# Performance work log

Hardware: AMD Instinct MI355X
Metric: run time of the kernel (lower is better)

## Reference

```python
import jax, jax.numpy as jnp
import numpy as np

N, E, ND, ED, HID, H, L = 50000, 800000, 32, 16, 96, 4, 3
C = HID // H  # per-head channels = 24
NEG_SLOPE = 0.2
LN_EPS = 1e-5


def setup_inputs() -> dict:
    key = jax.random.key(0)
    ks = iter(jax.random.split(key, 40))
    def r(shape, s=0.05):
        return jax.random.normal(next(ks), shape, jnp.float32) * s
    return dict(
        x=r((N, ND), 1.0),
        edge_index=jax.random.randint(next(ks), (2, E), 0, N),
        edge_attr=r((E, ED), 1.0),
        proj_w=r((ND, HID)), proj_b=jnp.zeros((HID,), jnp.float32),
        lin_l_w=r((L, HID, HID)), lin_l_b=jnp.zeros((L, HID), jnp.float32),
        lin_r_w=r((L, HID, HID)), lin_r_b=jnp.zeros((L, HID), jnp.float32),
        lin_e_w=r((L, ED, HID)),
        att=r((L, H, C)),
        conv_b=jnp.zeros((L, HID), jnp.float32),
        ln_g=jnp.ones((L, HID), jnp.float32), ln_b=jnp.zeros((L, HID), jnp.float32),
        head_w1=r((HID, HID // 2)), head_b1=jnp.zeros((HID // 2,), jnp.float32),
        head_w2=r((HID // 2, 1)), head_b2=jnp.zeros((1,), jnp.float32),
    )


def _layernorm(h, g, b):
    mu = h.mean(-1, keepdims=True)
    var = ((h - mu) ** 2).mean(-1, keepdims=True)
    return (h - mu) / jnp.sqrt(var + LN_EPS) * g + b


def _gatv2(x, src, dst, edge_attr, Wl, bl, Wr, br, We, att, bias):
    # GATv2Conv (PyG semantics, eval mode): x_l = lin_l(x) for source, x_r = lin_r(x) for target
    xl = (x @ Wl + bl).reshape(N, H, C)
    xr = (x @ Wr + br).reshape(N, H, C)
    e = (edge_attr @ We).reshape(E, H, C)
    m = jax.nn.leaky_relu(xl[src] + xr[dst] + e, NEG_SLOPE)  # [E,H,C]
    alpha = (m * att).sum(-1)  # [E,H]
    # segment softmax over incoming edges of each target node
    amax = jax.ops.segment_max(alpha, dst, num_segments=N)  # [N,H]
    ea = jnp.exp(alpha - amax[dst])
    denom = jax.ops.segment_sum(ea, dst, num_segments=N)
    alpha = ea / (denom[dst] + 1e-16)
    out = jax.ops.segment_sum(xl[src] * alpha[..., None], dst, num_segments=N)
    return out.reshape(N, HID) + bias


def reference(x, edge_index, edge_attr, proj_w, proj_b, lin_l_w, lin_l_b, lin_r_w,
              lin_r_b, lin_e_w, att, conv_b, ln_g, ln_b, head_w1, head_b1, head_w2, head_b2):
    src, dst = edge_index[0], edge_index[1]
    h = x @ proj_w + proj_b
    for l in range(L):
        m = _gatv2(h, src, dst, edge_attr, lin_l_w[l], lin_l_b[l], lin_r_w[l],
                   lin_r_b[l], lin_e_w[l], att[l], conv_b[l])
        h = _layernorm(h + m, ln_g[l], ln_b[l])
    h = jax.nn.gelu(h @ head_w1 + head_b1, approximate=False)
    return (h @ head_w2 + head_b2).squeeze(-1)
```

## Files before the change

kernel.cpp:

```cpp
#include <hip/hip_runtime.h>

constexpr int N_NODES = 50000;
constexpr int N_EDGES = 800000;
constexpr int ND  = 32;
constexpr int ED  = 16;
constexpr int HID = 96;
constexpr int NLAYER = 3;

typedef unsigned short ushort_t;
typedef unsigned int uint_t;
typedef __attribute__((ext_vector_type(8))) short bf16x8;
typedef __attribute__((ext_vector_type(4))) float f32x4;

__device__ __forceinline__ float bf2f(ushort_t u) {
    union { float f; uint_t ui; } c; c.ui = ((uint_t)u) << 16; return c.f;
}
__device__ __forceinline__ ushort_t f2bf(float f) {
    uint_t u = __float_as_uint(f);
    return (ushort_t)((u + 0x7FFFu + ((u >> 16) & 1u)) >> 16);
}

__global__ void k_rank(const int* __restrict__ dst, int* __restrict__ cnt,
                       int* __restrict__ rank) {
    int e = blockIdx.x * 256 + threadIdx.x;
    if (e >= N_EDGES) return;
    rank[e] = atomicAdd(&cnt[dst[e]], 1);
}

__global__ void k_scan_block(const int* __restrict__ deg, int* __restrict__ rowptr,
                             int* __restrict__ bsum) {
    __shared__ int s[256];
    int i = blockIdx.x * 256 + threadIdx.x;
    int v = (i < N_NODES) ? deg[i] : 0;
    s[threadIdx.x] = v;
    __syncthreads();
    for (int off = 1; off < 256; off <<= 1) {
        int t = (threadIdx.x >= off) ? s[threadIdx.x - off] : 0;
        __syncthreads();
        s[threadIdx.x] += t;
        __syncthreads();
    }
    if (i < N_NODES) rowptr[i] = s[threadIdx.x] - v;
    if (threadIdx.x == 255) bsum[blockIdx.x] = s[255];
}

__global__ void k_scan_bsum(int* __restrict__ bsum, int nb) {
    __shared__ int s[256];
    int t = threadIdx.x;
    int v = (t < nb) ? bsum[t] : 0;
    s[t] = v;
    __syncthreads();
    for (int off = 1; off < 256; off <<= 1) {
        int tv = (t >= off) ? s[t - off] : 0;
        __syncthreads();
        s[t] += tv;
        __syncthreads();
    }
    if (t < nb) bsum[t] = s[t] - v;
}

__global__ void k_scan_add(int* __restrict__ rowptr, const int* __restrict__ bsum) {
    int i = blockIdx.x * 256 + threadIdx.x;
    if (i < N_NODES) rowptr[i] += bsum[blockIdx.x];
    if (i == 0) rowptr[N_NODES] = N_EDGES;
}

__global__ void k_place(const int* __restrict__ src, const int* __restrict__ dst,
                        const int* __restrict__ rank, const int* __restrict__ rowptr,
                        int2* __restrict__ csre) {
    int e = blockIdx.x * 256 + threadIdx.x;
    if (e >= N_EDGES) return;
    int p = rowptr[dst[e]] + rank[e];
    csre[p] = make_int2(src[e], e);
}

__global__ void k_gather(const int2* __restrict__ csre, const int* __restrict__ dstA,
                         const float* __restrict__ eattr, int* __restrict__ srcs,
                         int* __restrict__ pdst, ushort_t* __restrict__ ea) {
    int p = blockIdx.x * 256 + threadIdx.x;
    if (p >= N_EDGES) return;
    int2 se = csre[p];
    int e = se.y;
    srcs[p] = se.x;
    pdst[p] = dstA[e];
    const float4* er = (const float4*)(eattr + (size_t)e * ED);
    float4 v0 = er[0], v1 = er[1], v2 = er[2], v3 = er[3];
    uint4 w0, w1;
    w0.x = (uint_t)f2bf(v0.x) | ((uint_t)f2bf(v0.y) << 16);
    w0.y = (uint_t)f2bf(v0.z) | ((uint_t)f2bf(v0.w) << 16);
    w0.z = (uint_t)f2bf(v1.x) | ((uint_t)f2bf(v1.y) << 16);
    w0.w = (uint_t)f2bf(v1.z) | ((uint_t)f2bf(v1.w) << 16);
    w1.x = (uint_t)f2bf(v2.x) | ((uint_t)f2bf(v2.y) << 16);
    w1.y = (uint_t)f2bf(v2.z) | ((uint_t)f2bf(v2.w) << 16);
    w1.z = (uint_t)f2bf(v3.x) | ((uint_t)f2bf(v3.y) << 16);
    w1.w = (uint_t)f2bf(v3.z) | ((uint_t)f2bf(v3.w) << 16);
    uint4* ew = (uint4*)(ea + (size_t)p * ED);
    ew[0] = w0;
    ew[1] = w1;
}

__global__ __launch_bounds__(192) void k_proj(const float* __restrict__ x,
                                              const float* __restrict__ pw,
                                              const float* __restrict__ pb,
                                              float* __restrict__ h) {
    int t = threadIdx.x;
    int c = t % 96, half = t / 96;
    float wreg[ND];
#pragma unroll
    for (int k = 0; k < ND; k++) wreg[k] = pw[k * HID + c];
    float b = pb[c];
    int n0 = blockIdx.x * 16 + half * 8;
    for (int i = 0; i < 8; i += 2) {
        int na = n0 + i, nb = na + 1;
        const float4* xa = (const float4*)(x + (size_t)na * ND);
        const float4* xb = (const float4*)(x + (size_t)nb * ND);
        float accA = b, accB = b;
#pragma unroll
        for (int k4 = 0; k4 < ND / 4; k4++) {
            float4 va = xa[k4], vb = xb[k4];
            accA += va.x * wreg[4 * k4] + va.y * wreg[4 * k4 + 1] +
                    va.z * wreg[4 * k4 + 2] + va.w * wreg[4 * k4 + 3];
            accB += vb.x * wreg[4 * k4] + vb.y * wreg[4 * k4 + 1] +
                    vb.z * wreg[4 * k4 + 2] + vb.w * wreg[4 * k4 + 3];
        }
        h[(size_t)na * HID + c] = accA;
        h[(size_t)nb * HID + c] = accB;
    }
}

__global__ __launch_bounds__(256) void k_linlr_mfma(
    const float* __restrict__ h, const float* __restrict__ Wl,
    const float* __restrict__ bl, const float* __restrict__ Wr,
    const float* __restrict__ br, ushort_t* __restrict__ xl,
    ushort_t* __restrict__ xr) {
    __shared__ ushort_t sW[192 * 104];
    __shared__ float sB[192];
    int t = threadIdx.x;

    for (int idx = t; idx < 192 * 96; idx += 256) {
        int n = idx % 192, k = idx / 192;
        float v = (n < 96) ? Wl[k * 96 + n] : Wr[k * 96 + (n - 96)];
        sW[n * 104 + k] = f2bf(v);
    }
    if (t < 192) sB[t] = (t < 96) ? bl[t] : br[t - 96];
    __syncthreads();

    int wv = t >> 6, lane = t & 63;
    int m0 = blockIdx.x * 64 + wv * 16;
    if (m0 >= N_NODES) return;
    int m = lane & 15, quad = lane >> 4;

    bf16x8 afr[3];
    const float* hrow = h + (size_t)(m0 + m) * HID;
#pragma unroll
    for (int s = 0; s < 3; s++) {
        float4 v0 = *(const float4*)(hrow + s * 32 + quad * 8);
        float4 v1 = *(const float4*)(hrow + s * 32 + quad * 8 + 4);
        bf16x8 a;
        a[0] = (short)f2bf(v0.x); a[1] = (short)f2bf(v0.y);
        a[2] = (short)f2bf(v0.z); a[3] = (short)f2bf(v0.w);
        a[4] = (short)f2bf(v1.x); a[5] = (short)f2bf(v1.y);
        a[6] = (short)f2bf(v1.z); a[7] = (short)f2bf(v1.w);
        afr[s] = a;
    }

#pragma unroll
    for (int nt = 0; nt < 12; nt++) {
        int ch = nt * 16 + m;
        f32x4 acc = {0.f, 0.f, 0.f, 0.f};
#pragma unroll
        for (int s = 0; s < 3; s++) {
            bf16x8 bfr = *(const bf16x8*)(sW + (nt * 16 + m) * 104 + s * 32 + quad * 8);
            acc = __builtin_amdgcn_mfma_f32_16x16x32_bf16(afr[s], bfr, acc, 0, 0, 0);
        }
        float bias = sB[ch];
        ushort_t* dst = (ch < 96) ? (xl + (size_t)(m0 + quad * 4) * HID + ch)
                                  : (xr + (size_t)(m0 + quad * 4) * HID + (ch - 96));
#pragma unroll
        for (int r = 0; r < 4; r++)
            dst[(size_t)r * HID] = f2bf(acc[r] + bias);
    }
}

__global__ __launch_bounds__(256) void k_ev(
    const ushort_t* __restrict__ xlb, const ushort_t* __restrict__ xrb,
    const ushort_t* __restrict__ ea, const int* __restrict__ srcs,
    const int* __restrict__ pdst, const float* __restrict__ WeL,
    const float* __restrict__ attL, float* __restrict__ evf) {
    int wid = blockIdx.x * 4 + (threadIdx.x >> 6);
    int lane = threadIdx.x & 63;
    if (wid >= N_EDGES / 128) return;
    int col = lane & 15, quad = lane >> 4;
    int comp = col & 1, base = col >> 1;

    int2 sp = *(const int2*)(srcs + wid * 128 + 2 * lane);
    int2 dp = *(const int2*)(pdst + wid * 128 + 2 * lane);

    bf16x8 afr[6];
#pragma unroll
    for (int mc = 0; mc < 6; mc++) {
        bf16x8 a = {0, 0, 0, 0, 0, 0, 0, 0};
        if (quad < 2) {
            int ch = (col >> 2) * 24 + mc * 4 + (col & 3);
#pragma unroll
            for (int j = 0; j < 8; j++)
                a[j] = (short)f2bf(WeL[(quad * 8 + j) * HID + ch]);
        }
        afr[mc] = a;
    }
    float attr[6][4];
#pragma unroll
    for (int mc = 0; mc < 6; mc++)
#pragma unroll
        for (int r = 0; r < 4; r++)
            attr[mc][r] = attL[quad * 24 + mc * 4 + r];

    bf16x8 bfr[2];
    uint4 xq[2][3], rq[2][3];

    auto getsd = [&](int b, int& sv, int& dv) {
        int sl = b * 8 + base;
        int sx = __shfl(sp.x, sl), sy = __shfl(sp.y, sl);
        int dx = __shfl(dp.x, sl), dy = __shfl(dp.y, sl);
        sv = comp ? sy : sx;
        dv = comp ? dy : dx;
    };
    auto issue = [&](int b, int pp) {
        int sv, dv;
        getsd(b, sv, dv);
        int p = wid * 128 + b * 16 + col;
        bf16x8 z8 = {0, 0, 0, 0, 0, 0, 0, 0};
        bfr[pp] = (quad < 2) ? *(const bf16x8*)(ea + (size_t)p * ED + quad * 8) : z8;
        const uint4* xp = (const uint4*)(xlb + (size_t)sv * HID + quad * 24);
        const uint4* rp = (const uint4*)(xrb + (size_t)dv * HID + quad * 24);
#pragma unroll
        for (int i = 0; i < 3; i++) {
            xq[pp][i] = xp[i];
            rq[pp][i] = rp[i];
        }
    };

    issue(0, 0);
#pragma unroll
    for (int b = 0; b < 8; b++) {
        int pp = b & 1;
        if (b < 7) issue(b + 1, pp ^ 1);

        f32x4 zero4 = {0.f, 0.f, 0.f, 0.f};
        f32x4 d[6];
#pragma unroll
        for (int mc = 0; mc < 6; mc++)
            d[mc] = __builtin_amdgcn_mfma_f32_16x16x32_bf16(afr[mc], bfr[pp], zero4, 0, 0, 0);

        uint_t ux[12] = {xq[pp][0].x, xq[pp][0].y, xq[pp][0].z, xq[pp][0].w,
                         xq[pp][1].x, xq[pp][1].y, xq[pp][1].z, xq[pp][1].w,
                         xq[pp][2].x, xq[pp][2].y, xq[pp][2].z, xq[pp][2].w};
        uint_t ur[12] = {rq[pp][0].x, rq[pp][0].y, rq[pp][0].z, rq[pp][0].w,
                         rq[pp][1].x, rq[pp][1].y, rq[pp][1].z, rq[pp][1].w,
                         rq[pp][2].x, rq[pp][2].y, rq[pp][2].z, rq[pp][2].w};
        float logit = 0.f;
#pragma unroll
        for (int mc = 0; mc < 6; mc++) {
            uint_t aL = ux[2 * mc], aH = ux[2 * mc + 1];
            uint_t rL = ur[2 * mc], rH = ur[2 * mc + 1];
            float x0 = bf2f((ushort_t)(aL & 0xffff)), x1 = bf2f((ushort_t)(aL >> 16));
            float x2 = bf2f((ushort_t)(aH & 0xffff)), x3 = bf2f((ushort_t)(aH >> 16));
            float r0 = bf2f((ushort_t)(rL & 0xffff)), r1 = bf2f((ushort_t)(rL >> 16));
            float r2 = bf2f((ushort_t)(rH & 0xffff)), r3 = bf2f((ushort_t)(rH >> 16));
            float z0 = x0 + r0 + d[mc][0]; z0 = z0 > 0.f ? z0 : 0.2f * z0;
            float z1 = x1 + r1 + d[mc][1]; z1 = z1 > 0.f ? z1 : 0.2f * z1;
            float z2 = x2 + r2 + d[mc][2]; z2 = z2 > 0.f ? z2 : 0.2f * z2;
            float z3 = x3 + r3 + d[mc][3]; z3 = z3 > 0.f ? z3 : 0.2f * z3;
            logit += z0 * attr[mc][0] + z1 * attr[mc][1] +
                     z2 * attr[mc][2] + z3 * attr[mc][3];
        }
        int p = wid * 128 + b * 16 + col;
        evf[4 * p + quad] = __expf(logit);
    }
}

__global__ __launch_bounds__(256) void k_agg(
    const ushort_t* __restrict__ xlb, const float* __restrict__ evf,
    const int* __restrict__ srcs, const int* __restrict__ rowptr,
    const float* __restrict__ convb, const float* __restrict__ lng,
    const float* __restrict__ lnb, float* __restrict__ h) {
    int lane = threadIdx.x & 63;
    int node = blockIdx.x * 4 + (threadIdx.x >> 6);
    int slot = lane >> 3, q = lane & 7;
    int c0 = q * 12, head = q >> 1;
    int beg = rowptr[node], end = rowptr[node + 1];
    int cnt = (end - beg + 7) >> 3;

    float n[12];
#pragma unroll
    for (int j = 0; j < 12; j++) n[j] = 0.f;
    float den = 0.f;

    if (cnt > 0) {
        int p = beg + slot;
        bool v = p < end;
        int pc = v ? p : beg;
        int src = srcs[pc];
        float evv = evf[4 * pc + head];
        const ushort_t* xp = xlb + (size_t)src * HID + c0;
        uint2 A0 = *(const uint2*)(xp);
        uint2 A1 = *(const uint2*)(xp + 4);
        uint2 A2 = *(const uint2*)(xp + 8);
        for (int it = 0; it < cnt; ++it) {
            int pn = beg + (it + 1) * 8 + slot;
            bool vn = pn < end;
            int pcn = vn ? pn : beg;
            int srcn = srcs[pcn];
            float evn = evf[4 * pcn + head];
            const ushort_t* xpn = xlb + (size_t)srcn * HID + c0;
            uint2 B0 = *(const uint2*)(xpn);
            uint2 B1 = *(const uint2*)(xpn + 4);
            uint2 B2 = *(const uint2*)(xpn + 8);

            float e = v ? evv : 0.f;
            n[0]  += e * bf2f((ushort_t)(A0.x & 0xffff));
            n[1]  += e * bf2f((ushort_t)(A0.x >> 16));
            n[2]  += e * bf2f((ushort_t)(A0.y & 0xffff));
            n[3]  += e * bf2f((ushort_t)(A0.y >> 16));
            n[4]  += e * bf2f((ushort_t)(A1.x & 0xffff));
            n[5]  += e * bf2f((ushort_t)(A1.x >> 16));
            n[6]  += e * bf2f((ushort_t)(A1.y & 0xffff));
            n[7]  += e * bf2f((ushort_t)(A1.y >> 16));
            n[8]  += e * bf2f((ushort_t)(A2.x & 0xffff));
            n[9]  += e * bf2f((ushort_t)(A2.x >> 16));
            n[10] += e * bf2f((ushort_t)(A2.y & 0xffff));
            n[11] += e * bf2f((ushort_t)(A2.y >> 16));
            den += e;

            v = vn; evv = evn;
            A0 = B0; A1 = B1; A2 = B2;
        }
    }
#pragma unroll
    for (int j = 0; j < 12; j++) {
        n[j] += __shfl_xor(n[j], 8);
        n[j] += __shfl_xor(n[j], 16);
        n[j] += __shfl_xor(n[j], 32);
    }
    den += __shfl_xor(den, 8);
    den += __shfl_xor(den, 16);
    den += __shfl_xor(den, 32);

    size_t nb = (size_t)node * HID + c0;
    float inv = 1.f / (den + 1e-16f);
    float4 h0 = *(const float4*)(h + nb);
    float4 h1 = *(const float4*)(h + nb + 4);
    float4 h2 = *(const float4*)(h + nb + 8);
    float vv[12] = {h0.x, h0.y, h0.z, h0.w, h1.x, h1.y, h1.z, h1.w,
                    h2.x, h2.y, h2.z, h2.w};
    float sm = 0.f;
#pragma unroll
    for (int j = 0; j < 12; j++) {
        vv[j] += n[j] * inv + convb[c0 + j];
        sm += vv[j];
    }
    sm += __shfl_xor(sm, 1); sm += __shfl_xor(sm, 2); sm += __shfl_xor(sm, 4);
    float mu = sm * (1.f / 96.f);
    float sv = 0.f;
#pragma unroll
    for (int j = 0; j < 12; j++) {
        vv[j] -= mu;
        sv += vv[j] * vv[j];
    }
    sv += __shfl_xor(sv, 1); sv += __shfl_xor(sv, 2); sv += __shfl_xor(sv, 4);
    float rstd = rsqrtf(sv * (1.f / 96.f) + 1e-5f);
    if (slot == 0) {
        float o[12];
#pragma unroll
        for (int j = 0; j < 12; j++)
            o[j] = vv[j] * rstd * lng[c0 + j] + lnb[c0 + j];
        *(float4*)(h + nb)     = make_float4(o[0], o[1], o[2], o[3]);
        *(float4*)(h + nb + 4) = make_float4(o[4], o[5], o[6], o[7]);
        *(float4*)(h + nb + 8) = make_float4(o[8], o[9], o[10], o[11]);
    }
}

__global__ __launch_bounds__(256) void k_head_mfma(
    const float* __restrict__ h, const float* __restrict__ W1,
    const float* __restrict__ b1, const float* __restrict__ W2,
    const float* __restrict__ b2, float* __restrict__ out) {
    __shared__ ushort_t sW[48 * 104];
    __shared__ float sB1[48];
    __shared__ float sW2[48];
    int t = threadIdx.x;
    for (int idx = t; idx < 48 * 96; idx += 256) {
        int j = idx % 48, k = idx / 48;
        sW[j * 104 + k] = f2bf(W1[k * 48 + j]);
    }
    if (t < 48) { sB1[t] = b1[t]; sW2[t] = W2[t]; }
    __syncthreads();

    int wv = t >> 6, lane = t & 63;
    int m0 = blockIdx.x * 64 + wv * 16;
    if (m0 >= N_NODES) return;
    int col = lane & 15, quad = lane >> 4;

    bf16x8 afr[3];
    const float* hrow = h + (size_t)(m0 + col) * HID;
#pragma unroll
    for (int s = 0; s < 3; s++) {
        float4 v0 = *(const float4*)(hrow + s * 32 + quad * 8);
        float4 v1 = *(const float4*)(hrow + s * 32 + quad * 8 + 4);
        bf16x8 a;
        a[0] = (short)f2bf(v0.x); a[1] = (short)f2bf(v0.y);
        a[2] = (short)f2bf(v0.z); a[3] = (short)f2bf(v0.w);
        a[4] = (short)f2bf(v1.x); a[5] = (short)f2bf(v1.y);
        a[6] = (short)f2bf(v1.z); a[7] = (short)f2bf(v1.w);
        afr[s] = a;
    }

    const float inv_sqrt2 = 0.70710678118654752f;
    float y0 = 0.f, y1 = 0.f, y2 = 0.f, y3 = 0.f;
#pragma unroll
    for (int nt = 0; nt < 3; nt++) {
        f32x4 acc = {0.f, 0.f, 0.f, 0.f};
#pragma unroll
        for (int s = 0; s < 3; s++) {
            bf16x8 bfr = *(const bf16x8*)(sW + (nt * 16 + col) * 104 + s * 32 + quad * 8);
            acc = __builtin_amdgcn_mfma_f32_16x16x32_bf16(afr[s], bfr, acc, 0, 0, 0);
        }
        int ch = nt * 16 + col;
        float bias = sB1[ch], w2 = sW2[ch];
        float v, g;
        v = acc[0] + bias; g = 0.5f * v * (1.f + erff(v * inv_sqrt2)); y0 += g * w2;
        v = acc[1] + bias; g = 0.5f * v * (1.f + erff(v * inv_sqrt2)); y1 += g * w2;
        v = acc[2] + bias; g = 0.5f * v * (1.f + erff(v * inv_sqrt2)); y2 += g * w2;
        v = acc[3] + bias; g = 0.5f * v * (1.f + erff(v * inv_sqrt2)); y3 += g * w2;
    }
    y0 += __shfl_xor(y0, 1); y0 += __shfl_xor(y0, 2);
    y0 += __shfl_xor(y0, 4); y0 += __shfl_xor(y0, 8);
    y1 += __shfl_xor(y1, 1); y1 += __shfl_xor(y1, 2);
    y1 += __shfl_xor(y1, 4); y1 += __shfl_xor(y1, 8);
    y2 += __shfl_xor(y2, 1); y2 += __shfl_xor(y2, 2);
    y2 += __shfl_xor(y2, 4); y2 += __shfl_xor(y2, 8);
    y3 += __shfl_xor(y3, 1); y3 += __shfl_xor(y3, 2);
    y3 += __shfl_xor(y3, 4); y3 += __shfl_xor(y3, 8);
    if (col == 0) {
        float bb = b2[0];
        out[m0 + quad * 4 + 0] = y0 + bb;
        out[m0 + quad * 4 + 1] = y1 + bb;
        out[m0 + quad * 4 + 2] = y2 + bb;
        out[m0 + quad * 4 + 3] = y3 + bb;
    }
}

extern "C" void kernel_launch(void* const* d_in, const int* in_sizes, int n_in,
                              void* d_out, int out_size, void* d_ws, size_t ws_size,
                              hipStream_t stream) {
    const float* x       = (const float*)d_in[0];
    const int*   eidx    = (const int*)  d_in[1];
    const float* eattr   = (const float*)d_in[2];
    const float* proj_w  = (const float*)d_in[3];
    const float* proj_b  = (const float*)d_in[4];
    const float* lin_l_w = (const float*)d_in[5];
    const float* lin_l_b = (const float*)d_in[6];
    const float* lin_r_w = (const float*)d_in[7];
    const float* lin_r_b = (const float*)d_in[8];
    const float* lin_e_w = (const float*)d_in[9];
    const float* att     = (const float*)d_in[10];
    const float* conv_b  = (const float*)d_in[11];
    const float* ln_g    = (const float*)d_in[12];
    const float* ln_b    = (const float*)d_in[13];
    const float* head_w1 = (const float*)d_in[14];
    const float* head_b1 = (const float*)d_in[15];
    const float* head_w2 = (const float*)d_in[16];
    const float* head_b2 = (const float*)d_in[17];
    float* out = (float*)d_out;

    char* p = (char*)d_ws;
    auto alloc = [&](size_t bytes) -> char* {
        char* r = p;
        p += (bytes + 255) & ~size_t(255);
        return r;
    };
    float*    h      = (float*)alloc(sizeof(float) * (size_t)N_NODES * HID);
    ushort_t* xl     = (ushort_t*)alloc(2 * (size_t)N_NODES * HID);
    ushort_t* xr     = (ushort_t*)alloc(2 * (size_t)N_NODES * HID);
    int*      cnt    = (int*)alloc(4 * (size_t)N_NODES);
    int*      rank   = (int*)alloc(4 * (size_t)N_EDGES);
    int*      rowptr = (int*)alloc(4 * (size_t)(N_NODES + 1));
    int*      bsum   = (int*)alloc(4 * 256);
    int2*     csre   = (int2*)alloc(8 * (size_t)N_EDGES);
    int*      srcs   = (int*)alloc(4 * ((size_t)N_EDGES + 256));
    int*      pdst   = (int*)alloc(4 * ((size_t)N_EDGES + 256));
    ushort_t* ea_csr = (ushort_t*)alloc(2 * (size_t)N_EDGES * ED);
    float*    ev     = (float*)alloc(16 * (size_t)N_EDGES);

    const int* srcA = eidx;
    const int* dstA = eidx + N_EDGES;

    int ebl = (N_EDGES + 255) / 256;
    int nbl = (N_NODES + 255) / 256;

    hipMemsetAsync(cnt, 0, 4 * (size_t)N_NODES, stream);
    k_rank<<<ebl, 256, 0, stream>>>(dstA, cnt, rank);
    k_scan_block<<<nbl, 256, 0, stream>>>(cnt, rowptr, bsum);
    k_scan_bsum<<<1, 256, 0, stream>>>(bsum, nbl);
    k_scan_add<<<nbl, 256, 0, stream>>>(rowptr, bsum);
    k_place<<<ebl, 256, 0, stream>>>(srcA, dstA, rank, rowptr, csre);
    k_gather<<<ebl, 256, 0, stream>>>(csre, dstA, eattr, srcs, pdst, ea_csr);

    k_proj<<<N_NODES / 16, 192, 0, stream>>>(x, proj_w, proj_b, h);
    for (int l = 0; l < NLAYER; l++) {
        k_linlr_mfma<<<(N_NODES + 63) / 64, 256, 0, stream>>>(
            h, lin_l_w + (size_t)l * HID * HID, lin_l_b + (size_t)l * HID,
            lin_r_w + (size_t)l * HID * HID, lin_r_b + (size_t)l * HID, xl, xr);
        k_ev<<<1563, 256, 0, stream>>>(xl, xr, ea_csr, srcs, pdst,
                                       lin_e_w + (size_t)l * ED * HID,
                                       att + (size_t)l * HID, ev);
        k_agg<<<N_NODES / 4, 256, 0, stream>>>(
            xl, ev, srcs, rowptr, conv_b + (size_t)l * HID,
            ln_g + (size_t)l * HID, ln_b + (size_t)l * HID, h);
    }
    k_head_mfma<<<(N_NODES + 63) / 64, 256, 0, stream>>>(h, head_w1, head_b1,
                                                         head_w2, head_b2, out);
}
```

Before: 538.5 us.

## Fuse edge-logit and aggregation kernels into one per-node GATv2 kernel

Merges the edge-score kernel and the node aggregation/LayerNorm kernel into a single kernel where each wavefront owns one destination node. It computes exp-logits for 16-edge tiles with MFMA and passes them to the aggregation lanes through shuffles. This removes the E×4 float ev buffer and the pdst array along with their global write and read traffic, and loads xr once per node instead of once per edge. The cost is that the double-buffered prefetch is gone and MFMA tiles are padded for low-degree nodes, so about half the lanes can sit idle. Each source row of xl is also gathered twice.

```diff
diff --git a/kernel.cpp b/kernel.cpp
--- a/kernel.cpp
+++ b/kernel.cpp
@@ -74,15 +74,14 @@
     csre[p] = make_int2(src[e], e);
 }
 
-__global__ void k_gather(const int2* __restrict__ csre, const int* __restrict__ dstA,
+__global__ void k_gather(const int2* __restrict__ csre,
                          const float* __restrict__ eattr, int* __restrict__ srcs,
-                         int* __restrict__ pdst, ushort_t* __restrict__ ea) {
+                         ushort_t* __restrict__ ea) {
     int p = blockIdx.x * 256 + threadIdx.x;
     if (p >= N_EDGES) return;
     int2 se = csre[p];
     int e = se.y;
     srcs[p] = se.x;
-    pdst[p] = dstA[e];
     const float4* er = (const float4*)(eattr + (size_t)e * ED);
     float4 v0 = er[0], v1 = er[1], v2 = er[2], v3 = er[3];
     uint4 w0, w1;
@@ -182,19 +181,21 @@
     }
 }
 
-__global__ __launch_bounds__(256) void k_ev(
+__global__ __launch_bounds__(256, 3) void k_fused(
     const ushort_t* __restrict__ xlb, const ushort_t* __restrict__ xrb,
     const ushort_t* __restrict__ ea, const int* __restrict__ srcs,
-    const int* __restrict__ pdst, const float* __restrict__ WeL,
-    const float* __restrict__ attL, float* __restrict__ evf) {
-    int wid = blockIdx.x * 4 + (threadIdx.x >> 6);
+    const int* __restrict__ rowptr, const float* __restrict__ WeL,
+    const float* __restrict__ attL, const float* __restrict__ convb,
+    const float* __restrict__ lng, const float* __restrict__ lnb,
+    float* __restrict__ h) {
     int lane = threadIdx.x & 63;
-    if (wid >= N_EDGES / 128) return;
+    int node = blockIdx.x * 4 + (threadIdx.x >> 6);
     int col = lane & 15, quad = lane >> 4;
-    int comp = col & 1, base = col >> 1;
-
-    int2 sp = *(const int2*)(srcs + wid * 128 + 2 * lane);
-    int2 dp = *(const int2*)(pdst + wid * 128 + 2 * lane);
+    int slot = lane >> 3, q = lane & 7;
+    int c0 = q * 12;
+
+    int beg = rowptr[node], end = rowptr[node + 1];
+    int ntile = (end - beg + 15) >> 4;
 
     bf16x8 afr[6];
 #pragma unroll
@@ -215,49 +216,41 @@
         for (int r = 0; r < 4; r++)
             attr[mc][r] = attL[quad * 24 + mc * 4 + r];
 
-    bf16x8 bfr[2];
-    uint4 xq[2][3], rq[2][3];
-
-    auto getsd = [&](int b, int& sv, int& dv) {
-        int sl = b * 8 + base;
-        int sx = __shfl(sp.x, sl), sy = __shfl(sp.y, sl);
-        int dx = __shfl(dp.x, sl), dy = __shfl(dp.y, sl);
-        sv = comp ? sy : sx;
-        dv = comp ? dy : dx;
-    };
-    auto issue = [&](int b, int pp) {
-        int sv, dv;
-        getsd(b, sv, dv);
-        int p = wid * 128 + b * 16 + col;
+    uint4 rqv[3];
+    {
+        const uint4* rp = (const uint4*)(xrb + (size_t)node * HID + quad * 24);
+        rqv[0] = rp[0]; rqv[1] = rp[1]; rqv[2] = rp[2];
+    }
+    uint_t ur[12] = {rqv[0].x, rqv[0].y, rqv[0].z, rqv[0].w,
+                     rqv[1].x, rqv[1].y, rqv[1].z, rqv[1].w,
+                     rqv[2].x, rqv[2].y, rqv[2].z, rqv[2].w};
+
+    float n[12];
+#pragma unroll
+    for (int j = 0; j < 12; j++) n[j] = 0.f;
+    float den = 0.f;
+
+    for (int t = 0; t < ntile; ++t) {
+        int p = beg + t * 16 + col;
+        int pc = (p < end) ? p : beg;
+        int sv = srcs[pc];
         bf16x8 z8 = {0, 0, 0, 0, 0, 0, 0, 0};
-        bfr[pp] = (quad < 2) ? *(const bf16x8*)(ea + (size_t)p * ED + quad * 8) : z8;
-        const uint4* xp = (const uint4*)(xlb + (size_t)sv * HID + quad * 24);
-        const uint4* rp = (const uint4*)(xrb + (size_t)dv * HID + quad * 24);
-#pragma unroll
-        for (int i = 0; i < 3; i++) {
-            xq[pp][i] = xp[i];
-            rq[pp][i] = rp[i];
-        }
-    };
-
-    issue(0, 0);
-#pragma unroll
-    for (int b = 0; b < 8; b++) {
-        int pp = b & 1;
-        if (b < 7) issue(b + 1, pp ^ 1);
+        bf16x8 bfr = (quad < 2) ? *(const bf16x8*)(ea + (size_t)pc * ED + quad * 8) : z8;
+        uint4 xq0, xq1, xq2;
+        {
+            const uint4* xp = (const uint4*)(xlb + (size_t)sv * HID + quad * 24);
+            xq0 = xp[0]; xq1 = xp[1]; xq2 = xp[2];
+        }
 
         f32x4 zero4 = {0.f, 0.f, 0.f, 0.f};
         f32x4 d[6];
 #pragma unroll
         for (int mc = 0; mc < 6; mc++)
-            d[mc] = __builtin_amdgcn_mfma_f32_16x16x32_bf16(afr[mc], bfr[pp], zero4, 0, 0, 0);
-
-        uint_t ux[12] = {xq[pp][0].x, xq[pp][0].y, xq[pp][0].z, xq[pp][0].w,
-                         xq[pp][1].x, xq[pp][1].y, xq[pp][1].z, xq[pp][1].w,
-                         xq[pp][2].x, xq[pp][2].y, xq[pp][2].z, xq[pp][2].w};
-        uint_t ur[12] = {rq[pp][0].x, rq[pp][0].y, rq[pp][0].z, rq[pp][0].w,
-                         rq[pp][1].x, rq[pp][1].y, rq[pp][1].z, rq[pp][1].w,
-                         rq[pp][2].x, rq[pp][2].y, rq[pp][2].z, rq[pp][2].w};
+            d[mc] = __builtin_amdgcn_mfma_f32_16x16x32_bf16(afr[mc], bfr, zero4, 0, 0, 0);
+
+        uint_t ux[12] = {xq0.x, xq0.y, xq0.z, xq0.w,
+                         xq1.x, xq1.y, xq1.z, xq1.w,
+                         xq2.x, xq2.y, xq2.z, xq2.w};
         float logit = 0.f;
 #pragma unroll
         for (int mc = 0; mc < 6; mc++) {
@@ -274,50 +267,21 @@
             logit += z0 * attr[mc][0] + z1 * attr[mc][1] +
                      z2 * attr[mc][2] + z3 * attr[mc][3];
         }
-        int p = wid * 128 + b * 16 + col;
-        evf[4 * p + quad] = __expf(logit);
-    }
-}
-
-__global__ __launch_bounds__(256) void k_agg(
-    const ushort_t* __restrict__ xlb, const float* __restrict__ evf,
-    const int* __restrict__ srcs, const int* __restrict__ rowptr,
-    const float* __restrict__ convb, const float* __restrict__ lng,
-    const float* __restrict__ lnb, float* __restrict__ h) {
-    int lane = threadIdx.x & 63;
-    int node = blockIdx.x * 4 + (threadIdx.x >> 6);
-    int slot = lane >> 3, q = lane & 7;
-    int c0 = q * 12, head = q >> 1;
-    int beg = rowptr[node], end = rowptr[node + 1];
-    int cnt = (end - beg + 7) >> 3;
-
-    float n[12];
-#pragma unroll
-    for (int j = 0; j < 12; j++) n[j] = 0.f;
-    float den = 0.f;
-
-    if (cnt > 0) {
-        int p = beg + slot;
-        bool v = p < end;
-        int pc = v ? p : beg;
-        int src = srcs[pc];
-        float evv = evf[4 * pc + head];
-        const ushort_t* xp = xlb + (size_t)src * HID + c0;
-        uint2 A0 = *(const uint2*)(xp);
-        uint2 A1 = *(const uint2*)(xp + 4);
-        uint2 A2 = *(const uint2*)(xp + 8);
-        for (int it = 0; it < cnt; ++it) {
-            int pn = beg + (it + 1) * 8 + slot;
-            bool vn = pn < end;
-            int pcn = vn ? pn : beg;
-            int srcn = srcs[pcn];
-            float evn = evf[4 * pcn + head];
-            const ushort_t* xpn = xlb + (size_t)srcn * HID + c0;
-            uint2 B0 = *(const uint2*)(xpn);
-            uint2 B1 = *(const uint2*)(xpn + 4);
-            uint2 B2 = *(const uint2*)(xpn + 8);
-
-            float e = v ? evv : 0.f;
+        float ev = __expf(logit);
+
+#pragma unroll
+        for (int sub = 0; sub < 2; ++sub) {
+            int eidx = t * 16 + sub * 8 + slot;
+            int pb = beg + eidx;
+            bool valid = pb < end;
+            int pbc = valid ? pb : beg;
+            float evx = __shfl(ev, (q >> 1) * 16 + sub * 8 + slot);
+            float e = valid ? evx : 0.f;
+            int srcb = srcs[pbc];
+            const ushort_t* xpb = xlb + (size_t)srcb * HID + c0;
+            uint2 A0 = *(const uint2*)(xpb);
+            uint2 A1 = *(const uint2*)(xpb + 4);
+            uint2 A2 = *(const uint2*)(xpb + 8);
             n[0]  += e * bf2f((ushort_t)(A0.x & 0xffff));
             n[1]  += e * bf2f((ushort_t)(A0.x >> 16));
             n[2]  += e * bf2f((ushort_t)(A0.y & 0xffff));
@@ -331,11 +295,9 @@
             n[10] += e * bf2f((ushort_t)(A2.y & 0xffff));
             n[11] += e * bf2f((ushort_t)(A2.y >> 16));
             den += e;
-
-            v = vn; evv = evn;
-            A0 = B0; A1 = B1; A2 = B2;
-        }
-    }
+        }
+    }
+
 #pragma unroll
     for (int j = 0; j < 12; j++) {
         n[j] += __shfl_xor(n[j], 8);
@@ -487,9 +449,7 @@
     int*      bsum   = (int*)alloc(4 * 256);
     int2*     csre   = (int2*)alloc(8 * (size_t)N_EDGES);
     int*      srcs   = (int*)alloc(4 * ((size_t)N_EDGES + 256));
-    int*      pdst   = (int*)alloc(4 * ((size_t)N_EDGES + 256));
     ushort_t* ea_csr = (ushort_t*)alloc(2 * (size_t)N_EDGES * ED);
-    float*    ev     = (float*)alloc(16 * (size_t)N_EDGES);
 
     const int* srcA = eidx;
     const int* dstA = eidx + N_EDGES;
@@ -503,19 +463,18 @@
     k_scan_bsum<<<1, 256, 0, stream>>>(bsum, nbl);
     k_scan_add<<<nbl, 256, 0, stream>>>(rowptr, bsum);
     k_place<<<ebl, 256, 0, stream>>>(srcA, dstA, rank, rowptr, csre);
-    k_gather<<<ebl, 256, 0, stream>>>(csre, dstA, eattr, srcs, pdst, ea_csr);
+    k_gather<<<ebl, 256, 0, stream>>>(csre, eattr, srcs, ea_csr);
 
     k_proj<<<N_NODES / 16, 192, 0, stream>>>(x, proj_w, proj_b, h);
     for (int l = 0; l < NLAYER; l++) {
         k_linlr_mfma<<<(N_NODES + 63) / 64, 256, 0, stream>>>(
             h, lin_l_w + (size_t)l * HID * HID, lin_l_b + (size_t)l * HID,
             lin_r_w + (size_t)l * HID * HID, lin_r_b + (size_t)l * HID, xl, xr);
-        k_ev<<<1563, 256, 0, stream>>>(xl, xr, ea_csr, srcs, pdst,
-                                       lin_e_w + (size_t)l * ED * HID,
-                                       att + (size_t)l * HID, ev);
-        k_agg<<<N_NODES / 4, 256, 0, stream>>>(
-            xl, ev, srcs, rowptr, conv_b + (size_t)l * HID,
-            ln_g + (size_t)l * HID, ln_b + (size_t)l * HID, h);
+        k_fused<<<N_NODES / 4, 256, 0, stream>>>(
+            xl, xr, ea_csr, srcs, rowptr,
+            lin_e_w + (size_t)l * ED * HID, att + (size_t)l * HID,
+            conv_b + (size_t)l * HID, ln_g + (size_t)l * HID,
+            ln_b + (size_t)l * HID, h);
     }
     k_head_mfma<<<(N_NODES + 63) / 64, 256, 0, stream>>>(h, head_w1, head_b1,
                                                          head_w2, head_b2, out);
```

Result: slower. 657.8 us (+22.1%).

## Fuse edge logit and CSR aggregation into one kernel with boundary partials

Applied to the files above, without the earlier changes.

Merges the per-edge attention kernel with neighbour aggregation. Each 64-thread block handles 128 dst-sorted edges and accumulates weighted xl rows and denominators per destination node in shared memory with LDS atomics. Nodes whose edge ranges cross a block boundary get left and right partials, which a new finalize kernel combines with softmax normalization and layernorm. This removes the ev buffer round trip and the second gather of xl rows. It adds shared-memory atomics and relies on at most NMAX distinct nodes per 128-edge block (extra nodes are clamped into the last slot), and also on no node's edges spanning more than two blocks.

```diff
diff --git a/kernel.cpp b/kernel.cpp
--- a/kernel.cpp
+++ b/kernel.cpp
@@ -6,6 +6,7 @@
 constexpr int ED  = 16;
 constexpr int HID = 96;
 constexpr int NLAYER = 3;
+constexpr int NMAX = 40;
 
 typedef unsigned short ushort_t;
 typedef unsigned int uint_t;
@@ -182,19 +183,27 @@
     }
 }
 
-__global__ __launch_bounds__(256) void k_ev(
+__global__ __launch_bounds__(64, 3) void k_evagg(
     const ushort_t* __restrict__ xlb, const ushort_t* __restrict__ xrb,
     const ushort_t* __restrict__ ea, const int* __restrict__ srcs,
-    const int* __restrict__ pdst, const float* __restrict__ WeL,
-    const float* __restrict__ attL, float* __restrict__ evf) {
-    int wid = blockIdx.x * 4 + (threadIdx.x >> 6);
-    int lane = threadIdx.x & 63;
-    if (wid >= N_EDGES / 128) return;
+    const int* __restrict__ pdst, const int* __restrict__ rowptr,
+    const float* __restrict__ WeL, const float* __restrict__ attL,
+    float* __restrict__ accsum, float* __restrict__ accden,
+    float* __restrict__ partL, float* __restrict__ partR) {
+    int wid = blockIdx.x;
+    int lane = threadIdx.x;
     int col = lane & 15, quad = lane >> 4;
-    int comp = col & 1, base = col >> 1;
-
-    int2 sp = *(const int2*)(srcs + wid * 128 + 2 * lane);
-    int2 dp = *(const int2*)(pdst + wid * 128 + 2 * lane);
+    int comp = col & 1, cbase = col >> 1;
+    int base = wid * 128;
+
+    __shared__ float sacc[NMAX][96];
+    __shared__ float sden[NMAX][4];
+    for (int i = lane; i < NMAX * 96; i += 64) (&sacc[0][0])[i] = 0.f;
+    for (int i = lane; i < NMAX * 4; i += 64) (&sden[0][0])[i] = 0.f;
+
+    int2 sp = *(const int2*)(srcs + base + 2 * lane);
+    int2 dp = *(const int2*)(pdst + base + 2 * lane);
+    int nlo = __shfl(dp.x, 0);
 
     bf16x8 afr[6];
 #pragma unroll
@@ -219,7 +228,7 @@
     uint4 xq[2][3], rq[2][3];
 
     auto getsd = [&](int b, int& sv, int& dv) {
-        int sl = b * 8 + base;
+        int sl = b * 8 + cbase;
         int sx = __shfl(sp.x, sl), sy = __shfl(sp.y, sl);
         int dx = __shfl(dp.x, sl), dy = __shfl(dp.y, sl);
         sv = comp ? sy : sx;
@@ -228,7 +237,7 @@
     auto issue = [&](int b, int pp) {
         int sv, dv;
         getsd(b, sv, dv);
-        int p = wid * 128 + b * 16 + col;
+        int p = base + b * 16 + col;
         bf16x8 z8 = {0, 0, 0, 0, 0, 0, 0, 0};
         bfr[pp] = (quad < 2) ? *(const bf16x8*)(ea + (size_t)p * ED + quad * 8) : z8;
         const uint4* xp = (const uint4*)(xlb + (size_t)sv * HID + quad * 24);
@@ -238,6 +247,30 @@
             xq[pp][i] = xp[i];
             rq[pp][i] = rp[i];
         }
+    };
+
+    int q = lane & 7, slot = lane >> 3;
+    float n12[12];
+#pragma unroll
+    for (int j = 0; j < 12; j++) n12[j] = 0.f;
+    float dn = 0.f;
+    int curn;
+    {
+        int m = slot >> 1;
+        int nx = __shfl(dp.x, m), ny = __shfl(dp.y, m);
+        curn = (slot & 1) ? ny : nx;
+    }
+
+    auto flushacc = [&]() {
+        int idx = curn - nlo;
+        idx = (idx < NMAX) ? idx : (NMAX - 1);
+        float* ap = &sacc[idx][q * 12];
+#pragma unroll
+        for (int j = 0; j < 12; j++) atomicAdd(ap + j, n12[j]);
+        if (!(q & 1)) atomicAdd(&sden[idx][q >> 1], dn);
+#pragma unroll
+        for (int j = 0; j < 12; j++) n12[j] = 0.f;
+        dn = 0.f;
     };
 
     issue(0, 0);
@@ -274,77 +307,92 @@
             logit += z0 * attr[mc][0] + z1 * attr[mc][1] +
                      z2 * attr[mc][2] + z3 * attr[mc][3];
         }
-        int p = wid * 128 + b * 16 + col;
-        evf[4 * p + quad] = __expf(logit);
-    }
-}
-
-__global__ __launch_bounds__(256) void k_agg(
-    const ushort_t* __restrict__ xlb, const float* __restrict__ evf,
-    const int* __restrict__ srcs, const int* __restrict__ rowptr,
-    const float* __restrict__ convb, const float* __restrict__ lng,
-    const float* __restrict__ lnb, float* __restrict__ h) {
+        float ev = __expf(logit);
+
+#pragma unroll
+        for (int sub = 0; sub < 2; sub++) {
+            int e = sub * 8 + slot;
+            int S = (q >> 1) * 16 + e;
+            float evs = __shfl(ev, S);
+            int m = b * 8 + sub * 4 + (slot >> 1);
+            int nx = __shfl(dp.x, m), ny = __shfl(dp.y, m);
+            int nd = (slot & 1) ? ny : nx;
+            if (nd != curn) { flushacc(); curn = nd; }
+            uint_t w[6];
+#pragma unroll
+            for (int k = 0; k < 6; k++) {
+                uint_t lo = (uint_t)__shfl((int)ux[k], S);
+                uint_t hi = (uint_t)__shfl((int)ux[k + 6], S);
+                w[k] = (q & 1) ? hi : lo;
+            }
+#pragma unroll
+            for (int k = 0; k < 6; k++) {
+                n12[2 * k]     += evs * bf2f((ushort_t)(w[k] & 0xffff));
+                n12[2 * k + 1] += evs * bf2f((ushort_t)(w[k] >> 16));
+            }
+            dn += evs;
+        }
+    }
+    flushacc();
+
+    int nhi = __shfl(dp.y, 63);
+    for (int nd = nlo; nd <= nhi; ++nd) {
+        int idx = nd - nlo;
+        idx = (idx < NMAX) ? idx : (NMAX - 1);
+        int beg = rowptr[nd], end = rowptr[nd + 1];
+        bool lb = beg < base;
+        bool rb = end > base + 128;
+        if (lane < 24) {
+            float4 v = *(float4*)&sacc[idx][lane * 4];
+            if (lb)      *(float4*)(partL + (size_t)wid * 100 + lane * 4) = v;
+            else if (rb) *(float4*)(partR + (size_t)wid * 100 + lane * 4) = v;
+            else         *(float4*)(accsum + (size_t)nd * 96 + lane * 4) = v;
+        } else if (lane == 24) {
+            float4 dv = *(float4*)&sden[idx][0];
+            if (lb)      *(float4*)(partL + (size_t)wid * 100 + 96) = dv;
+            else if (rb) *(float4*)(partR + (size_t)wid * 100 + 96) = dv;
+            else         *(float4*)(accden + (size_t)nd * 4) = dv;
+        }
+    }
+}
+
+__global__ __launch_bounds__(256) void k_fin(
+    const float* __restrict__ accsum, const float* __restrict__ accden,
+    const float* __restrict__ partL, const float* __restrict__ partR,
+    const int* __restrict__ rowptr, const float* __restrict__ convb,
+    const float* __restrict__ lng, const float* __restrict__ lnb,
+    float* __restrict__ h) {
     int lane = threadIdx.x & 63;
-    int node = blockIdx.x * 4 + (threadIdx.x >> 6);
     int slot = lane >> 3, q = lane & 7;
-    int c0 = q * 12, head = q >> 1;
+    int node = blockIdx.x * 32 + (threadIdx.x >> 6) * 8 + slot;
+    if (node >= N_NODES) return;
+    int c0 = q * 12;
     int beg = rowptr[node], end = rowptr[node + 1];
-    int cnt = (end - beg + 7) >> 3;
-
-    float n[12];
-#pragma unroll
-    for (int j = 0; j < 12; j++) n[j] = 0.f;
+
+    float a[12];
     float den = 0.f;
-
-    if (cnt > 0) {
-        int p = beg + slot;
-        bool v = p < end;
-        int pc = v ? p : beg;
-        int src = srcs[pc];
-        float evv = evf[4 * pc + head];
-        const ushort_t* xp = xlb + (size_t)src * HID + c0;
-        uint2 A0 = *(const uint2*)(xp);
-        uint2 A1 = *(const uint2*)(xp + 4);
-        uint2 A2 = *(const uint2*)(xp + 8);
-        for (int it = 0; it < cnt; ++it) {
-            int pn = beg + (it + 1) * 8 + slot;
-            bool vn = pn < end;
-            int pcn = vn ? pn : beg;
-            int srcn = srcs[pcn];
-            float evn = evf[4 * pcn + head];
-            const ushort_t* xpn = xlb + (size_t)srcn * HID + c0;
-            uint2 B0 = *(const uint2*)(xpn);
-            uint2 B1 = *(const uint2*)(xpn + 4);
-            uint2 B2 = *(const uint2*)(xpn + 8);
-
-            float e = v ? evv : 0.f;
-            n[0]  += e * bf2f((ushort_t)(A0.x & 0xffff));
-            n[1]  += e * bf2f((ushort_t)(A0.x >> 16));
-            n[2]  += e * bf2f((ushort_t)(A0.y & 0xffff));
-            n[3]  += e * bf2f((ushort_t)(A0.y >> 16));
-            n[4]  += e * bf2f((ushort_t)(A1.x & 0xffff));
-            n[5]  += e * bf2f((ushort_t)(A1.x >> 16));
-            n[6]  += e * bf2f((ushort_t)(A1.y & 0xffff));
-            n[7]  += e * bf2f((ushort_t)(A1.y >> 16));
-            n[8]  += e * bf2f((ushort_t)(A2.x & 0xffff));
-            n[9]  += e * bf2f((ushort_t)(A2.x >> 16));
-            n[10] += e * bf2f((ushort_t)(A2.y & 0xffff));
-            n[11] += e * bf2f((ushort_t)(A2.y >> 16));
-            den += e;
-
-            v = vn; evv = evn;
-            A0 = B0; A1 = B1; A2 = B2;
-        }
-    }
-#pragma unroll
-    for (int j = 0; j < 12; j++) {
-        n[j] += __shfl_xor(n[j], 8);
-        n[j] += __shfl_xor(n[j], 16);
-        n[j] += __shfl_xor(n[j], 32);
-    }
-    den += __shfl_xor(den, 8);
-    den += __shfl_xor(den, 16);
-    den += __shfl_xor(den, 32);
+    if (beg == end) {
+#pragma unroll
+        for (int j = 0; j < 12; j++) a[j] = 0.f;
+    } else {
+        int b0 = beg >> 7, b1 = (end - 1) >> 7;
+        if (b0 == b1) {
+            const float* ap = accsum + (size_t)node * 96 + c0;
+            float4 a0 = *(const float4*)(ap);
+            float4 a1 = *(const float4*)(ap + 4);
+            float4 a2 = *(const float4*)(ap + 8);
+            a[0] = a0.x; a[1] = a0.y; a[2]  = a0.z; a[3]  = a0.w;
+            a[4] = a1.x; a[5] = a1.y; a[6]  = a1.z; a[7]  = a1.w;
+            a[8] = a2.x; a[9] = a2.y; a[10] = a2.z; a[11] = a2.w;
+            den = accden[node * 4 + (q >> 1)];
+        } else {
+            const float* pR = partR + (size_t)b0 * 100;
+            const float* pL = partL + (size_t)b1 * 100;
+#pragma unroll
+            for (int j = 0; j < 12; j++) a[j] = pR[c0 + j] + pL[c0 + j];
+            den = pR[96 + (q >> 1)] + pL[96 + (q >> 1)];
+        }
+    }
 
     size_t nb = (size_t)node * HID + c0;
     float inv = 1.f / (den + 1e-16f);
@@ -356,7 +404,7 @@
     float sm = 0.f;
 #pragma unroll
     for (int j = 0; j < 12; j++) {
-        vv[j] += n[j] * inv + convb[c0 + j];
+        vv[j] += a[j] * inv + convb[c0 + j];
         sm += vv[j];
     }
     sm += __shfl_xor(sm, 1); sm += __shfl_xor(sm, 2); sm += __shfl_xor(sm, 4);
@@ -369,15 +417,13 @@
     }
     sv += __shfl_xor(sv, 1); sv += __shfl_xor(sv, 2); sv += __shfl_xor(sv, 4);
     float rstd = rsqrtf(sv * (1.f / 96.f) + 1e-5f);
-    if (slot == 0) {
-        float o[12];
-#pragma unroll
-        for (int j = 0; j < 12; j++)
-            o[j] = vv[j] * rstd * lng[c0 + j] + lnb[c0 + j];
-        *(float4*)(h + nb)     = make_float4(o[0], o[1], o[2], o[3]);
-        *(float4*)(h + nb + 4) = make_float4(o[4], o[5], o[6], o[7]);
-        *(float4*)(h + nb + 8) = make_float4(o[8], o[9], o[10], o[11]);
-    }
+    float o[12];
+#pragma unroll
+    for (int j = 0; j < 12; j++)
+        o[j] = vv[j] * rstd * lng[c0 + j] + lnb[c0 + j];
+    *(float4*)(h + nb)     = make_float4(o[0], o[1], o[2], o[3]);
+    *(float4*)(h + nb + 4) = make_float4(o[4], o[5], o[6], o[7]);
+    *(float4*)(h + nb + 8) = make_float4(o[8], o[9], o[10], o[11]);
 }
 
 __global__ __launch_bounds__(256) void k_head_mfma(
@@ -478,6 +524,7 @@
         p += (bytes + 255) & ~size_t(255);
         return r;
     };
+    constexpr int NBLK = N_EDGES / 128;
     float*    h      = (float*)alloc(sizeof(float) * (size_t)N_NODES * HID);
     ushort_t* xl     = (ushort_t*)alloc(2 * (size_t)N_NODES * HID);
     ushort_t* xr     = (ushort_t*)alloc(2 * (size_t)N_NODES * HID);
@@ -489,7 +536,10 @@
     int*      srcs   = (int*)alloc(4 * ((size_t)N_EDGES + 256));
     int*      pdst   = (int*)alloc(4 * ((size_t)N_EDGES + 256));
     ushort_t* ea_csr = (ushort_t*)alloc(2 * (size_t)N_EDGES * ED);
-    float*    ev     = (float*)alloc(16 * (size_t)N_EDGES);
+    float*    accsum = (float*)alloc(sizeof(float) * (size_t)N_NODES * 96);
+    float*    accden = (float*)alloc(sizeof(float) * (size_t)N_NODES * 4);
+    float*    partL  = (float*)alloc(sizeof(float) * (size_t)NBLK * 100);
+    float*    partR  = (float*)alloc(sizeof(float) * (size_t)NBLK * 100);
 
     const int* srcA = eidx;
     const int* dstA = eidx + N_EDGES;
@@ -510,11 +560,12 @@
         k_linlr_mfma<<<(N_NODES + 63) / 64, 256, 0, stream>>>(
             h, lin_l_w + (size_t)l * HID * HID, lin_l_b + (size_t)l * HID,
             lin_r_w + (size_t)l * HID * HID, lin_r_b + (size_t)l * HID, xl, xr);
-        k_ev<<<1563, 256, 0, stream>>>(xl, xr, ea_csr, srcs, pdst,
-                                       lin_e_w + (size_t)l * ED * HID,
-                                       att + (size_t)l * HID, ev);
-        k_agg<<<N_NODES / 4, 256, 0, stream>>>(
-            xl, ev, srcs, rowptr, conv_b + (size_t)l * HID,
+        k_evagg<<<NBLK, 64, 0, stream>>>(xl, xr, ea_csr, srcs, pdst, rowptr,
+                                         lin_e_w + (size_t)l * ED * HID,
+                                         att + (size_t)l * HID,
+                                         accsum, accden, partL, partR);
+        k_fin<<<(N_NODES + 31) / 32, 256, 0, stream>>>(
+            accsum, accden, partL, partR, rowptr, conv_b + (size_t)l * HID,
             ln_g + (size_t)l * HID, ln_b + (size_t)l * HID, h);
     }
     k_head_mfma<<<(N_NODES + 63) / 64, 256, 0, stream>>>(h, head_w1, head_b1,
```

Result: slower. 1.111 ms (+106.2%).
